# Kernel optimization log

Measured on AMD Instinct MI355X. Metric: run time of the kernel, lower is better.

## Reference

```python
import jax, jax.numpy as jnp
import numpy as np

DT = 1.0          # ODENet default dt
W_SCALE = 0.05    # keep forward-Euler trajectory numerically tame


def setup_inputs() -> dict:
    key = jax.random.key(0)
    ks = jax.random.split(key, 4)
    T, B, H = 8192, 128, 128
    x = jax.random.normal(ks[0], (T, B, 1), dtype=jnp.float32)
    W1 = jax.random.normal(ks[1], (2, H), dtype=jnp.float32) * W_SCALE
    b1 = jnp.zeros((H,), dtype=jnp.float32)
    W2 = jax.random.normal(ks[2], (H, H), dtype=jnp.float32) * W_SCALE
    b2 = jnp.zeros((H,), dtype=jnp.float32)
    W3 = jax.random.normal(ks[3], (H, 1), dtype=jnp.float32) * W_SCALE
    b3 = jnp.zeros((1,), dtype=jnp.float32)
    return {"x": x, "W1": W1, "b1": b1, "W2": W2, "b2": b2, "W3": W3, "b3": b3}


def reference(x, W1, b1, W2, b2, W3, b3):
    # x: (T, B, 1). State y: (B,), init zeros (initial_value in ODENet.forward).
    # Forward Euler: y_{n+1} = y_n + dt * f(x_n, y_n), returning all T states
    # (y_0 included), i.e. output shape (T, B, 1) matching the input shape.
    x_sq = x[..., 0]                      # (T, B) == self.derivative_network.input
    B = x_sq.shape[1]
    y0 = jnp.zeros((B,), dtype=x.dtype)   # initial_value

    def deriv(xt, y):
        inp = jnp.stack([xt, y], axis=-1)          # (B, 2)
        h = jnp.tanh(inp @ W1 + b1)                # (B, H)
        h = jnp.tanh(h @ W2 + b2)                  # (B, H)
        return (h @ W3 + b3)[..., 0]               # (B,)

    def step(y, xt):
        y_next = y + DT * deriv(xt, y)
        return y_next, y_next

    # T-1 Euler steps produce states y_1..y_{T-1}
    _, ys = jax.lax.scan(step, y0, x_sq[:-1])      # (T-1, B)
    out = jnp.concatenate([y0[None], ys], axis=0)  # (T, B)
    return out[..., None]                          # (T, B, 1)
```

## Files before the change

kernel.cpp:

```cpp
#include <hip/hip_runtime.h>

#define T_STEPS 8192
#define BATCH   128
#define HID     128
#define NTHR    512

typedef float v2f __attribute__((ext_vector_type(2)));

__device__ __forceinline__ float fast_tanh(float z) {
    float e = __expf(2.0f * z);
    float r = __builtin_amdgcn_rcpf(1.0f + e);
    return fmaf(-2.0f, r, 1.0f);
}

__device__ __forceinline__ float quad_sum(float x) {
    int t1 = __builtin_amdgcn_update_dpp(0, __builtin_bit_cast(int, x),
                                         0xB1 , 0xf, 0xf, false);
    x += __builtin_bit_cast(float, t1);
    int t2 = __builtin_amdgcn_update_dpp(0, __builtin_bit_cast(int, x),
                                         0x4E , 0xf, 0xf, false);
    x += __builtin_bit_cast(float, t2);
    return x;
}

__device__ __forceinline__ float wave64_sum(float x) {
#define DPP_ADD(ctrl) do {                                                        \
        int t_ = __builtin_amdgcn_update_dpp(0, __builtin_bit_cast(int, x),       \
                                             (ctrl), 0xf, 0xf, false);            \
        x += __builtin_bit_cast(float, t_); } while (0)
    DPP_ADD(0x111); DPP_ADD(0x112); DPP_ADD(0x114);
    DPP_ADD(0x118); DPP_ADD(0x142); DPP_ADD(0x143);
#undef DPP_ADD
    int s_ = __builtin_amdgcn_readlane(__builtin_bit_cast(int, x), 63);
    return __builtin_bit_cast(float, s_);
}

__device__ __forceinline__ float bcast_lane(float v, int l) {
    int r = __builtin_amdgcn_readlane(__builtin_bit_cast(int, v), l);
    return __builtin_bit_cast(float, r);
}

#define FORALL16(M) M(0) M(1) M(2) M(3) M(4) M(5) M(6) M(7) \
                    M(8) M(9) M(10) M(11) M(12) M(13) M(14) M(15)

__global__ __launch_bounds__(NTHR, 2) void odenet_scan(
    const float* __restrict__ x,
    const float* __restrict__ W1, const float* __restrict__ b1,
    const float* __restrict__ W2, const float* __restrict__ b2,
    const float* __restrict__ W3, const float* __restrict__ b3,
    float* __restrict__ out) {

    const int b    = blockIdx.x;
    const int tid  = threadIdx.x;
    const int w    = tid >> 6;
    const int lane = tid & 63;
    const int j    = (w << 4) | (lane >> 2);
    const int s    = lane & 3;

    __shared__ __align__(16) float h1buf[8][144];
    __shared__ __align__(16) float dyx[2][8];

    const float* col = W2 + j;
    const int kb = s << 5;
#define DECLW(i) v2f wp##i = {col[(kb + 2*(i) + 0) * HID],                        \
                              col[(kb + 2*(i) + 1) * HID]};
    FORALL16(DECLW)
#undef DECLW
#define PINW(i) asm volatile("" : "+v"(wp##i));
    FORALL16(PINW)
#undef PINW

    float w1xa = W1[lane],      w1ya = W1[HID + lane],      b1a = b1[lane];
    float w1xb = W1[lane + 64], w1yb = W1[HID + lane + 64], b1b = b1[lane + 64];
    float b2j  = b2[j];
    float w3j4 = W3[j] * 0.25f;
    float b3v  = b3[0];
    asm volatile("" : "+v"(w1xa), "+v"(w1ya), "+v"(b1a),
                      "+v"(w1xb), "+v"(w1yb), "+v"(b1b),
                      "+v"(b2j), "+v"(w3j4), "+v"(b3v));

    float y    = 0.0f;
    float xbuf = 0.0f;
    float ybuf = 0.0f;
    if (tid == 0) out[b] = 0.0f;

    const float4* h4 = (const float4*)&h1buf[w][s * 36];

    for (int t = 0; t < T_STEPS - 1; ++t) {
        const int tm = t & 63;
        if (tm == 0)
            xbuf = x[(t + lane) * BATCH + b];
        float xv = bcast_lane(xbuf, tm);

        float ha = fast_tanh(fmaf(y, w1ya, fmaf(xv, w1xa, b1a)));
        float hb = fast_tanh(fmaf(y, w1yb, fmaf(xv, w1xb, b1b)));
        h1buf[w][((lane >> 5)    ) * 36 + (lane & 31)] = ha;
        h1buf[w][((lane >> 5) + 2) * 36 + (lane & 31)] = hb;

        v2f a0 = {0.f, 0.f}, a1 = {0.f, 0.f}, a2 = {0.f, 0.f}, a3 = {0.f, 0.f};
        {
            float4 q0 = h4[0], q1 = h4[1], q2 = h4[2], q3 = h4[3];
            float4 q4 = h4[4], q5 = h4[5], q6 = h4[6], q7 = h4[7];
            v2f h0 = {q0.x, q0.y}, h1_ = {q0.z, q0.w};
            v2f h2 = {q1.x, q1.y}, h3 = {q1.z, q1.w};
            v2f h4v = {q2.x, q2.y}, h5 = {q2.z, q2.w};
            v2f h6 = {q3.x, q3.y}, h7 = {q3.z, q3.w};
            v2f h8 = {q4.x, q4.y}, h9 = {q4.z, q4.w};
            v2f hA = {q5.x, q5.y}, hB = {q5.z, q5.w};
            v2f hC = {q6.x, q6.y}, hD = {q6.z, q6.w};
            v2f hE = {q7.x, q7.y}, hF = {q7.z, q7.w};
            a0 += wp0 * h0;  a1 += wp1 * h1_; a2 += wp2 * h2;  a3 += wp3 * h3;
            a0 += wp4 * h4v; a1 += wp5 * h5;  a2 += wp6 * h6;  a3 += wp7 * h7;
            a0 += wp8 * h8;  a1 += wp9 * h9;  a2 += wp10 * hA; a3 += wp11 * hB;
            a0 += wp12 * hC; a1 += wp13 * hD; a2 += wp14 * hE; a3 += wp15 * hF;
        }
        v2f ap = (a0 + a1) + (a2 + a3);

        float z2 = quad_sum(ap.x + ap.y);

        float h2 = fast_tanh(z2 + b2j);
        float dyw = wave64_sum(w3j4 * h2);

        if (lane == 0) dyx[t & 1][w] = dyw;
        __syncthreads();
        const float4* dx4 = (const float4*)dyx[t & 1];
        float4 r0 = dx4[0], r1 = dx4[1];
        y += ((r0.x + r0.y) + (r0.z + r0.w))
           + ((r1.x + r1.y) + (r1.z + r1.w)) + b3v;

        if (tid < 64) {
            ybuf = (lane == tm) ? y : ybuf;
            if (tm == 63)
                out[(t - 62 + lane) * BATCH + b] = ybuf;
        }
    }
    if (tid < 63)
        out[(T_STEPS - 63 + lane) * BATCH + b] = ybuf;
}

extern "C" void kernel_launch(void* const* d_in, const int* in_sizes, int n_in,
                              void* d_out, int out_size, void* d_ws, size_t ws_size,
                              hipStream_t stream) {
    const float* x  = (const float*)d_in[0];
    const float* W1 = (const float*)d_in[1];
    const float* b1 = (const float*)d_in[2];
    const float* W2 = (const float*)d_in[3];
    const float* b2 = (const float*)d_in[4];
    const float* W3 = (const float*)d_in[5];
    const float* b3 = (const float*)d_in[6];

    odenet_scan<<<dim3(BATCH), dim3(NTHR), 0, stream>>>(
        x, W1, b1, W2, b2, W3, b3, (float*)d_out);
}
```

Before: 4.022 ms.

## Prefetch next x chunk, precompute input term before barrier, trim wave reduction

The next step's x broadcast and the x*W1+b1 products are now computed before the barrier, so they overlap the wait and leave the post-barrier critical path shorter. The x chunk for the following 64 steps is prefetched one chunk early so the global load latency is hidden. The wave reduction drops the two intra-quad DPP stages, since values are already uniform within each quad after quad_sum, and uses the full W3 weight instead of a quarter. The __syncthreads is replaced by an inline-asm waitcnt plus barrier, and ybuf is now updated in every wave, which adds a little work per step.

```diff
diff --git a/kernel.cpp b/kernel.cpp
--- a/kernel.cpp
+++ b/kernel.cpp
@@ -23,13 +23,15 @@
     return x;
 }
 
-__device__ __forceinline__ float wave64_sum(float x) {
+__device__ __forceinline__ float wave_sum_quaduniform(float x) {
 #define DPP_ADD(ctrl) do {                                                        \
         int t_ = __builtin_amdgcn_update_dpp(0, __builtin_bit_cast(int, x),       \
                                              (ctrl), 0xf, 0xf, false);            \
         x += __builtin_bit_cast(float, t_); } while (0)
-    DPP_ADD(0x111); DPP_ADD(0x112); DPP_ADD(0x114);
-    DPP_ADD(0x118); DPP_ADD(0x142); DPP_ADD(0x143);
+    DPP_ADD(0x114);
+    DPP_ADD(0x118);
+    DPP_ADD(0x142);
+    DPP_ADD(0x143);
 #undef DPP_ADD
     int s_ = __builtin_amdgcn_readlane(__builtin_bit_cast(int, x), 63);
     return __builtin_bit_cast(float, s_);
@@ -72,28 +74,29 @@
 
     float w1xa = W1[lane],      w1ya = W1[HID + lane],      b1a = b1[lane];
     float w1xb = W1[lane + 64], w1yb = W1[HID + lane + 64], b1b = b1[lane + 64];
-    float b2j  = b2[j];
-    float w3j4 = W3[j] * 0.25f;
-    float b3v  = b3[0];
+    float b2j = b2[j], w3j = W3[j], b3v = b3[0];
     asm volatile("" : "+v"(w1xa), "+v"(w1ya), "+v"(b1a),
                       "+v"(w1xb), "+v"(w1yb), "+v"(b1b),
-                      "+v"(b2j), "+v"(w3j4), "+v"(b3v));
+                      "+v"(b2j), "+v"(w3j), "+v"(b3v));
 
     float y    = 0.0f;
-    float xbuf = 0.0f;
     float ybuf = 0.0f;
-    if (tid == 0) out[b] = 0.0f;
+    if (w == 0 && lane == 0) out[b] = 0.0f;
+
+    float xbuf  = x[lane * BATCH + b];
+    int   nb    = 64;
+    float xnext = x[min(nb + lane, T_STEPS - 1) * BATCH + b];
+    float xv = bcast_lane(xbuf, 0);
+    float ax = fmaf(xv, w1xa, b1a);
+    float bx = fmaf(xv, w1xb, b1b);
 
     const float4* h4 = (const float4*)&h1buf[w][s * 36];
 
     for (int t = 0; t < T_STEPS - 1; ++t) {
         const int tm = t & 63;
-        if (tm == 0)
-            xbuf = x[(t + lane) * BATCH + b];
-        float xv = bcast_lane(xbuf, tm);
 
-        float ha = fast_tanh(fmaf(y, w1ya, fmaf(xv, w1xa, b1a)));
-        float hb = fast_tanh(fmaf(y, w1yb, fmaf(xv, w1xb, b1b)));
+        float ha = fast_tanh(fmaf(y, w1ya, ax));
+        float hb = fast_tanh(fmaf(y, w1yb, bx));
         h1buf[w][((lane >> 5)    ) * 36 + (lane & 31)] = ha;
         h1buf[w][((lane >> 5) + 2) * 36 + (lane & 31)] = hb;
 
@@ -116,25 +119,36 @@
         }
         v2f ap = (a0 + a1) + (a2 + a3);
 
-        float z2 = quad_sum(ap.x + ap.y);
-
-        float h2 = fast_tanh(z2 + b2j);
-        float dyw = wave64_sum(w3j4 * h2);
+        float z2  = quad_sum(ap.x + ap.y);
+        float h2  = fast_tanh(z2 + b2j);
+        float dyw = wave_sum_quaduniform(w3j * h2);
 
         if (lane == 0) dyx[t & 1][w] = dyw;
-        __syncthreads();
+
+        const int tmn = (t + 1) & 63;
+        if (tmn == 0) {
+            xbuf = xnext;
+            nb += 64;
+            xnext = x[min(nb + lane, T_STEPS - 1) * BATCH + b];
+        }
+        float xvn = bcast_lane(xbuf, tmn);
+        float axn = fmaf(xvn, w1xa, b1a);
+        float bxn = fmaf(xvn, w1xb, b1b);
+
+        asm volatile("s_waitcnt lgkmcnt(0)\n\ts_barrier" ::: "memory");
+
         const float4* dx4 = (const float4*)dyx[t & 1];
         float4 r0 = dx4[0], r1 = dx4[1];
         y += ((r0.x + r0.y) + (r0.z + r0.w))
            + ((r1.x + r1.y) + (r1.z + r1.w)) + b3v;
 
-        if (tid < 64) {
-            ybuf = (lane == tm) ? y : ybuf;
-            if (tm == 63)
-                out[(t - 62 + lane) * BATCH + b] = ybuf;
-        }
+        ybuf = (lane == tm) ? y : ybuf;
+        if (w == 0 && tm == 63)
+            out[(t - 62 + lane) * BATCH + b] = ybuf;
+
+        ax = axn; bx = bxn;
     }
-    if (tid < 63)
+    if (w == 0 && lane < 63)
         out[(T_STEPS - 63 + lane) * BATCH + b] = ybuf;
 }
 
```

New measurement: 4.015 ms. Within noise of the previous version (-0.2%).
